# Kernel optimization log

Hardware: AMD Instinct MI355X
Metric: run time of the kernel (lower is better)

The kernel has to match this reference:

```python
import jax, jax.numpy as jnp
import numpy as np

EPS = 1e-12  # matches torch F.normalize default eps


def setup_inputs() -> dict:
    key = jax.random.key(0)
    k_h, = jax.random.split(key, 1)
    B, S, D = 4, 4096, 2048
    h = jax.random.normal(k_h, (B, S, D), dtype=jnp.float32)
    alpha = jnp.asarray(2.0, dtype=jnp.float32)  # alpha_init
    beta = jnp.asarray(0.5, dtype=jnp.float32)   # beta_init
    return {"h": h, "alpha": alpha, "beta": beta}


def reference(h, alpha, beta):
    # --- concentration: mean pairwise cosine similarity (off-diagonal) ---
    # F.normalize(h, dim=-1): x / max(||x||_2, eps)
    norm = jnp.linalg.norm(h, axis=-1, keepdims=True)
    h_norm = h / jnp.maximum(norm, EPS)
    # sim: (B, S, S) via batched GEMM, same as torch.bmm
    sim = jnp.einsum('bid,bjd->bij', h_norm, h_norm)
    B, S, _ = sim.shape
    # mean over all off-diagonal entries across the whole batch
    diag_sum = jnp.einsum('bii->', sim)
    denom = jnp.asarray(B * S * (S - 1), dtype=sim.dtype)
    conc = (jnp.sum(sim) - diag_sum) / denom
    lambda_t = jax.nn.sigmoid(alpha * (conc - beta))
    return (lambda_t, conc)
```

## Files before the change

kernel.cpp:

```cpp
#include <hip/hip_runtime.h>
#include <math.h>

#define NBATCH 4
#define SROWS  4096
#define DCOLS  2048
#define BPB    128
#define ROWS_PER_WAVE (SROWS / (BPB * 4))

__global__ __launch_bounds__(256, 2)
void row_normalize_sum(const float* __restrict__ h, double* __restrict__ s_acc) {
    const int b    = blockIdx.x >> 7;
    const int blk  = blockIdx.x & (BPB - 1);
    const int wave = threadIdx.x >> 6;
    const int lane = threadIdx.x & 63;

    const float* hb = h + (size_t)b * SROWS * DCOLS;
    const int wid      = blk * 4 + wave;
    const int row_base = wid * ROWS_PER_WAVE;

    float acc[32];
#pragma unroll
    for (int i = 0; i < 32; ++i) acc[i] = 0.0f;

    for (int r = 0; r < ROWS_PER_WAVE; r += 2) {
        const float4* p0 = (const float4*)(hb + (size_t)(row_base + r)     * DCOLS) + lane;
        const float4* p1 = (const float4*)(hb + (size_t)(row_base + r + 1) * DCOLS) + lane;
        float4 v0[8], v1[8];
#pragma unroll
        for (int s = 0; s < 8; ++s) v0[s] = p0[s * 64];
#pragma unroll
        for (int s = 0; s < 8; ++s) v1[s] = p1[s * 64];

        float ss0 = 0.0f, ss1 = 0.0f;
#pragma unroll
        for (int s = 0; s < 8; ++s) {
            ss0 += v0[s].x * v0[s].x + v0[s].y * v0[s].y + v0[s].z * v0[s].z + v0[s].w * v0[s].w;
            ss1 += v1[s].x * v1[s].x + v1[s].y * v1[s].y + v1[s].z * v1[s].z + v1[s].w * v1[s].w;
        }
#pragma unroll
        for (int m = 32; m >= 1; m >>= 1) {
            ss0 += __shfl_xor(ss0, m, 64);
            ss1 += __shfl_xor(ss1, m, 64);
        }
        const float inv0 = (float)(1.0 / fmax(sqrt((double)ss0), 1e-12));
        const float inv1 = (float)(1.0 / fmax(sqrt((double)ss1), 1e-12));
#pragma unroll
        for (int s = 0; s < 8; ++s) {
            acc[s * 4 + 0] += v0[s].x * inv0;
            acc[s * 4 + 1] += v0[s].y * inv0;
            acc[s * 4 + 2] += v0[s].z * inv0;
            acc[s * 4 + 3] += v0[s].w * inv0;
            acc[s * 4 + 0] += v1[s].x * inv1;
            acc[s * 4 + 1] += v1[s].y * inv1;
            acc[s * 4 + 2] += v1[s].z * inv1;
            acc[s * 4 + 3] += v1[s].w * inv1;
        }
    }

    __shared__ float red[4][DCOLS];
#pragma unroll
    for (int s = 0; s < 8; ++s) {
        float4* dst = (float4*)&red[wave][s * 256 + lane * 4];
        *dst = make_float4(acc[s * 4 + 0], acc[s * 4 + 1], acc[s * 4 + 2], acc[s * 4 + 3]);
    }
    __syncthreads();

#pragma unroll
    for (int k = 0; k < 8; ++k) {
        const int c = k * 256 + threadIdx.x;
        const double v = (double)red[0][c] + (double)red[1][c]
                       + (double)red[2][c] + (double)red[3][c];
        atomicAdd(&s_acc[(size_t)b * DCOLS + c], v);
    }
}

__global__ void finalize_kernel(const double* __restrict__ s_acc,
                                const float* __restrict__ alpha,
                                const float* __restrict__ beta,
                                float* __restrict__ out) {
    __shared__ double red[256];
    double ssq = 0.0;
    for (int i = threadIdx.x; i < NBATCH * DCOLS; i += 256) {
        const double v = s_acc[i];
        ssq += v * v;
    }
    red[threadIdx.x] = ssq;
    __syncthreads();
    for (int off = 128; off > 0; off >>= 1) {
        if (threadIdx.x < off) red[threadIdx.x] += red[threadIdx.x + off];
        __syncthreads();
    }
    if (threadIdx.x == 0) {
        const double num   = red[0] - (double)NBATCH * (double)SROWS;
        const double denom = (double)NBATCH * (double)SROWS * (double)(SROWS - 1);
        const double conc  = num / denom;
        const double a = (double)alpha[0];
        const double bt = (double)beta[0];
        const double lam = 1.0 / (1.0 + exp(-a * (conc - bt)));
        out[0] = (float)lam;
        out[1] = (float)conc;
    }
}

extern "C" void kernel_launch(void* const* d_in, const int* in_sizes, int n_in,
                              void* d_out, int out_size, void* d_ws, size_t ws_size,
                              hipStream_t stream) {
    (void)in_sizes; (void)n_in; (void)out_size; (void)ws_size;
    const float* h     = (const float*)d_in[0];
    const float* alpha = (const float*)d_in[1];
    const float* beta  = (const float*)d_in[2];
    float* out         = (float*)d_out;
    double* s_acc      = (double*)d_ws;

    hipMemsetAsync(s_acc, 0, (size_t)NBATCH * DCOLS * sizeof(double), stream);

    row_normalize_sum<<<NBATCH * BPB, 256, 0, stream>>>(h, s_acc);
    finalize_kernel<<<1, 256, 0, stream>>>(s_acc, alpha, beta, out);
}
```

Before: 205.1 us.

## Replace double atomics with per-block partials and a two-stage deterministic reduction

The main kernel now writes each block's per-column partial sums to a workspace buffer instead of issuing fp64 atomicAdds into a shared accumulator. A new reduction kernel sums the 128 partials per batch column, squares them and reduces per block, and the finalize kernel does a single-wave shuffle reduction. This removes atomic contention and the memset, at the cost of an extra kernel launch and about 4 MB of partial-buffer traffic. Partial sums per block are now accumulated in fp32 rather than fp64.

```diff
diff --git a/kernel.cpp b/kernel.cpp
--- a/kernel.cpp
+++ b/kernel.cpp
@@ -5,10 +5,13 @@
 #define SROWS  4096
 #define DCOLS  2048
 #define BPB    128
+#define NBLK1  (NBATCH * BPB)
 #define ROWS_PER_WAVE (SROWS / (BPB * 4))
 
+#define SSQ_OFFSET ((size_t)NBLK1 * DCOLS)
+
 __global__ __launch_bounds__(256, 2)
-void row_normalize_sum(const float* __restrict__ h, double* __restrict__ s_acc) {
+void row_normalize_sum(const float* __restrict__ h, float* __restrict__ part) {
     const int b    = blockIdx.x >> 7;
     const int blk  = blockIdx.x & (BPB - 1);
     const int wave = threadIdx.x >> 6;
@@ -65,36 +68,58 @@
     }
     __syncthreads();
 
+    float* dst = part + (size_t)blockIdx.x * DCOLS;
 #pragma unroll
     for (int k = 0; k < 8; ++k) {
         const int c = k * 256 + threadIdx.x;
-        const double v = (double)red[0][c] + (double)red[1][c]
-                       + (double)red[2][c] + (double)red[3][c];
-        atomicAdd(&s_acc[(size_t)b * DCOLS + c], v);
+        dst[c] = red[0][c] + red[1][c] + red[2][c] + red[3][c];
     }
 }
 
-__global__ void finalize_kernel(const double* __restrict__ s_acc,
+__global__ __launch_bounds__(256, 4)
+void reduce_partials(const float* __restrict__ part, double* __restrict__ ssq_part) {
+    const int b    = blockIdx.x >> 4;
+    const int c    = ((blockIdx.x & 15) * 128) + (threadIdx.x & 127);
+    const int half = threadIdx.x >> 7;
+    const float* pb = part + (size_t)b * BPB * DCOLS;
+
+    double sum = 0.0;
+    const int p0 = half * 64;
+#pragma unroll 8
+    for (int p = p0; p < p0 + 64; ++p)
+        sum += (double)pb[(size_t)p * DCOLS + c];
+
+    __shared__ double sh[256];
+    sh[threadIdx.x] = sum;
+    __syncthreads();
+
+    double ssq = 0.0;
+    if (threadIdx.x < 128) {
+        const double s = sh[threadIdx.x] + sh[threadIdx.x + 128];
+        ssq = s * s;
+    }
+    __syncthreads();
+    sh[threadIdx.x] = ssq;
+    __syncthreads();
+    for (int off = 64; off > 0; off >>= 1) {
+        if (threadIdx.x < off) sh[threadIdx.x] += sh[threadIdx.x + off];
+        __syncthreads();
+    }
+    if (threadIdx.x == 0) ssq_part[blockIdx.x] = sh[0];
+}
+
+__global__ void finalize_kernel(const double* __restrict__ ssq_part,
                                 const float* __restrict__ alpha,
                                 const float* __restrict__ beta,
                                 float* __restrict__ out) {
-    __shared__ double red[256];
-    double ssq = 0.0;
-    for (int i = threadIdx.x; i < NBATCH * DCOLS; i += 256) {
-        const double v = s_acc[i];
-        ssq += v * v;
-    }
-    red[threadIdx.x] = ssq;
-    __syncthreads();
-    for (int off = 128; off > 0; off >>= 1) {
-        if (threadIdx.x < off) red[threadIdx.x] += red[threadIdx.x + off];
-        __syncthreads();
-    }
+    double v = ssq_part[threadIdx.x];
+#pragma unroll
+    for (int m = 32; m >= 1; m >>= 1) v += __shfl_xor(v, m, 64);
     if (threadIdx.x == 0) {
-        const double num   = red[0] - (double)NBATCH * (double)SROWS;
+        const double num   = v - (double)NBATCH * (double)SROWS;
         const double denom = (double)NBATCH * (double)SROWS * (double)(SROWS - 1);
         const double conc  = num / denom;
-        const double a = (double)alpha[0];
+        const double a  = (double)alpha[0];
         const double bt = (double)beta[0];
         const double lam = 1.0 / (1.0 + exp(-a * (conc - bt)));
         out[0] = (float)lam;
@@ -110,10 +135,10 @@
     const float* alpha = (const float*)d_in[1];
     const float* beta  = (const float*)d_in[2];
     float* out         = (float*)d_out;
-    double* s_acc      = (double*)d_ws;
+    float* part        = (float*)d_ws;
+    double* ssq_part   = (double*)((float*)d_ws + SSQ_OFFSET);
 
-    hipMemsetAsync(s_acc, 0, (size_t)NBATCH * DCOLS * sizeof(double), stream);
-
-    row_normalize_sum<<<NBATCH * BPB, 256, 0, stream>>>(h, s_acc);
-    finalize_kernel<<<1, 256, 0, stream>>>(s_acc, alpha, beta, out);
+    row_normalize_sum<<<NBLK1, 256, 0, stream>>>(h, part);
+    reduce_partials<<<64, 256, 0, stream>>>(part, ssq_part);
+    finalize_kernel<<<1, 64, 0, stream>>>(ssq_part, alpha, beta, out);
 }
```

Result: faster. 200.0 us (-2.5%).
